# Performance work log

Measured on AMD Instinct MI355X. Metric: run time of the kernel, lower is better.

Reference implementation:

```python
import jax, jax.numpy as jnp
import numpy as np
from math import sqrt

B, C, L = 32, 32, 512            # batch, channels(enc_in), seq_len
INTRA, INTER = 1024, 256          # memory-bank intra_len, inter_len
DCP, DDE = 64, 512                # compress width (retrieved set size), denoise hidden
SCALE = 0.05


def setup_inputs() -> dict:
    key = jax.random.key(0)
    ks = jax.random.split(key, 12)
    s = 0.02  # small init scale for weights
    return {
        "x_loc": jax.random.normal(ks[0], (B, C, L), jnp.float32),
        "indices": jax.random.randint(ks[1], (B, L), 0, INTRA),
        "map_raw": jax.random.normal(ks[2], (C, INTRA, INTER), jnp.float32),
        # compress: Linear(INTER->DCP), ReLU, Linear(DCP->DCP)
        "cW1": jax.random.normal(ks[3], (DCP, INTER), jnp.float32) * s,
        "cb1": jnp.zeros((DCP,), jnp.float32),
        "cW2": jax.random.normal(ks[4], (DCP, DCP), jnp.float32) * s,
        "cb2": jnp.zeros((DCP,), jnp.float32),
        # denoise: Linear(INTRA->DDE), ReLU, Linear(DDE->INTRA)
        "dW1": jax.random.normal(ks[5], (DDE, INTRA), jnp.float32) * s,
        "db1": jnp.zeros((DDE,), jnp.float32),
        "dW2": jax.random.normal(ks[6], (INTRA, DDE), jnp.float32) * s,
        "db2": jnp.zeros((INTRA,), jnp.float32),
        "lamda1": jnp.zeros((C, 1), jnp.float32),
        "lamda2": jnp.zeros((1, L), jnp.float32),
    }


def reference(x_loc, indices, map_raw, cW1, cb1, cW2, cb2,
              dW1, db1, dW2, db2, lamda1, lamda2):
    # compress along inter_len: (C, INTRA, INTER) -> (C, INTRA, DCP)
    map_tmp = jax.nn.relu(map_raw @ cW1.T + cb1) @ cW2.T + cb2
    map_tmp = jnp.swapaxes(map_tmp, 1, 2)            # (C, DCP, INTRA)
    # denoise along intra_len
    map_st = jax.nn.relu(map_tmp @ dW1.T + db1) @ dW2.T + db2  # (C, DCP, INTRA)
    # gather: map_dy[b,c,d,l] = map_st[c, d, indices[b,l]]
    map_dy = jnp.transpose(map_st[:, :, indices], (2, 0, 1, 3))  # (B, C, DCP, L)
    # l1 similarity (negative L1 distance, scaled by sqrt(L))
    scores = -jnp.sum(jnp.abs(x_loc[:, :, None, :] - map_dy), axis=-1) / sqrt(L)  # (B,C,DCP)
    scores = jax.nn.softmax(scores * SCALE, axis=2)
    lamda = jax.nn.sigmoid(lamda1) @ jax.nn.sigmoid(lamda2)     # (C, L)
    x_global = jnp.einsum('bchl,bch->bcl', map_dy, scores)      # (B, C, L)
    return x_global * lamda + x_loc * (1.0 - lamda)
```

## Files before the change

kernel.cpp:

```cpp
#include <hip/hip_runtime.h>
#include <hip/hip_bf16.h>

#define Bn 32
#define Cn 32
#define Ln 512
#define INTRA 1024
#define INTER 256
#define DCP 64
#define DDE 512
#define SCALEF 0.05f

typedef __attribute__((ext_vector_type(8))) short short8;
typedef __attribute__((ext_vector_type(4))) float floatx4;

__device__ __forceinline__ short bf16_of(float f) {
    union { float f; unsigned u; } v; v.f = f;
    unsigned r = (v.u + 0x7FFFu + ((v.u >> 16) & 1u)) >> 16;
    return (short)r;
}
__device__ __forceinline__ float f_of_bf16(short h) {
    union { unsigned u; float f; } v;
    v.u = ((unsigned)(unsigned short)h) << 16;
    return v.f;
}

__global__ __launch_bounds__(256) void prep_weights(
    const float* __restrict__ cW1, const float* __restrict__ cW2,
    const float* __restrict__ dW1, const float* __restrict__ dW2,
    short* __restrict__ cW1b, short* __restrict__ cW2b,
    short* __restrict__ dW1b, short* __restrict__ dW2b)
{
    int i = blockIdx.x * 256 + threadIdx.x;
    if (i < 64 * 256) cW1b[i] = bf16_of(cW1[i]);
    if (i < 64 * 64)  cW2b[i] = bf16_of(cW2[i]);
    if (i < DDE * INTRA) { dW1b[i] = bf16_of(dW1[i]); dW2b[i] = bf16_of(dW2[i]); }
}

__global__ __launch_bounds__(256) void compress_fused(
    const float* __restrict__ map_raw, const short* __restrict__ cW1b,
    const float* __restrict__ cb1, const short* __restrict__ cW2b,
    const float* __restrict__ cb2, short* __restrict__ M1T)
{
    const int c  = blockIdx.y;
    const int m0 = blockIdx.x * 64;
    const float* A = map_raw + (long)c * INTRA * INTER + (long)m0 * INTER;

    __shared__ short lds[64 * 32 + 64 * 32 + 64 * 64];
    short* Asb = lds;
    short* Bsb = lds + 2048;
    short* Tsb = lds + 4096;

    const int t    = threadIdx.x;
    const int w    = t >> 6;
    const int lane = t & 63;
    const int ln   = lane & 15;
    const int quad = lane >> 4;
    const int sr = t >> 2;
    const int sk = (t & 3) * 8;

    floatx4 acc[4] = {};

    float4 a0 = *(const float4*)(A + sr * INTER + sk);
    float4 a1 = *(const float4*)(A + sr * INTER + sk + 4);
    short8 bpre = *(const short8*)(cW1b + sr * INTER + sk);

    for (int k0 = 0; k0 < INTER; k0 += 32) {
        __syncthreads();
        short8 av;
        av[0] = bf16_of(a0.x); av[1] = bf16_of(a0.y);
        av[2] = bf16_of(a0.z); av[3] = bf16_of(a0.w);
        av[4] = bf16_of(a1.x); av[5] = bf16_of(a1.y);
        av[6] = bf16_of(a1.z); av[7] = bf16_of(a1.w);
        *(short8*)&Asb[sr * 32 + sk] = av;
        *(short8*)&Bsb[sr * 32 + sk] = bpre;
        __syncthreads();

        if (k0 + 32 < INTER) {
            a0 = *(const float4*)(A + sr * INTER + k0 + 32 + sk);
            a1 = *(const float4*)(A + sr * INTER + k0 + 32 + sk + 4);
            bpre = *(const short8*)(cW1b + sr * INTER + k0 + 32 + sk);
        }

        short8 af = *(const short8*)&Asb[(w * 16 + ln) * 32 + quad * 8];
        #pragma unroll
        for (int nt = 0; nt < 4; ++nt) {
            short8 bf = *(const short8*)&Bsb[(nt * 16 + ln) * 32 + quad * 8];
            acc[nt] = __builtin_amdgcn_mfma_f32_16x16x32_bf16(af, bf, acc[nt], 0, 0, 0);
        }
    }

    __syncthreads();

    #pragma unroll
    for (int nt = 0; nt < 4; ++nt) {
        const int n = nt * 16 + ln;
        const float b = cb1[n];
        #pragma unroll
        for (int r = 0; r < 4; ++r) {
            const int m = w * 16 + quad * 4 + r;
            Tsb[m * 64 + n] = bf16_of(fmaxf(acc[nt][r] + b, 0.f));
        }
    }
    {
        const int n = t >> 2, kc = (t & 3) * 16;
        *(short8*)&lds[n * 64 + kc]     = *(const short8*)(cW2b + n * 64 + kc);
        *(short8*)&lds[n * 64 + kc + 8] = *(const short8*)(cW2b + n * 64 + kc + 8);
    }
    __syncthreads();

    floatx4 acc2[4] = {};
    #pragma unroll
    for (int ks = 0; ks < 2; ++ks) {
        short8 af = *(const short8*)&Tsb[(w * 16 + ln) * 64 + ks * 32 + quad * 8];
        #pragma unroll
        for (int nt = 0; nt < 4; ++nt) {
            short8 bf = *(const short8*)&lds[(nt * 16 + ln) * 64 + ks * 32 + quad * 8];
            acc2[nt] = __builtin_amdgcn_mfma_f32_16x16x32_bf16(af, bf, acc2[nt], 0, 0, 0);
        }
    }

    short* outp = M1T + (long)c * 64 * INTRA;
    #pragma unroll
    for (int nt = 0; nt < 4; ++nt) {
        const int n = nt * 16 + ln;
        const float b = cb2[n];
        short t0 = bf16_of(acc2[nt][0] + b);
        short t1 = bf16_of(acc2[nt][1] + b);
        short t2 = bf16_of(acc2[nt][2] + b);
        short t3 = bf16_of(acc2[nt][3] + b);
        const int m = m0 + w * 16 + quad * 4;
        *(short4*)(outp + (long)n * INTRA + m) = make_short4(t0, t1, t2, t3);
    }
}

__global__ __launch_bounds__(256) void gemm_dn1(
    const short* __restrict__ A, const short* __restrict__ M1T,
    const float* __restrict__ db1, short* __restrict__ HT)
{
    const int c  = blockIdx.y;
    const int m0 = blockIdx.x * 64;
    const short* Bc = M1T + (long)c * 64 * INTRA;

    __shared__ short Asb[64 * 72];
    __shared__ short Bsb[64 * 72];

    const int t = threadIdx.x, w = t >> 6, lane = t & 63;
    const int ln = lane & 15, quad = lane >> 4;
    const int sr = t >> 2, sk = (t & 3) * 16;

    floatx4 acc[4] = {};
    short8 a0 = *(const short8*)(A + (long)(m0 + sr) * INTRA + sk);
    short8 a1 = *(const short8*)(A + (long)(m0 + sr) * INTRA + sk + 8);
    short8 b0 = *(const short8*)(Bc + (long)sr * INTRA + sk);
    short8 b1 = *(const short8*)(Bc + (long)sr * INTRA + sk + 8);

    for (int k0 = 0; k0 < INTRA; k0 += 64) {
        __syncthreads();
        *(short8*)&Asb[sr * 72 + sk]     = a0;
        *(short8*)&Asb[sr * 72 + sk + 8] = a1;
        *(short8*)&Bsb[sr * 72 + sk]     = b0;
        *(short8*)&Bsb[sr * 72 + sk + 8] = b1;
        __syncthreads();
        const int kn = k0 + 64;
        if (kn < INTRA) {
            a0 = *(const short8*)(A + (long)(m0 + sr) * INTRA + kn + sk);
            a1 = *(const short8*)(A + (long)(m0 + sr) * INTRA + kn + sk + 8);
            b0 = *(const short8*)(Bc + (long)sr * INTRA + kn + sk);
            b1 = *(const short8*)(Bc + (long)sr * INTRA + kn + sk + 8);
        }
        short8 af0 = *(const short8*)&Asb[(w * 16 + ln) * 72 + quad * 8];
        short8 af1 = *(const short8*)&Asb[(w * 16 + ln) * 72 + 32 + quad * 8];
        #pragma unroll
        for (int nt = 0; nt < 4; ++nt) {
            short8 bf0 = *(const short8*)&Bsb[(nt * 16 + ln) * 72 + quad * 8];
            short8 bf1 = *(const short8*)&Bsb[(nt * 16 + ln) * 72 + 32 + quad * 8];
            acc[nt] = __builtin_amdgcn_mfma_f32_16x16x32_bf16(af0, bf0, acc[nt], 0, 0, 0);
            acc[nt] = __builtin_amdgcn_mfma_f32_16x16x32_bf16(af1, bf1, acc[nt], 0, 0, 0);
        }
    }

    float bm[4];
    #pragma unroll
    for (int r = 0; r < 4; ++r) bm[r] = db1[m0 + w * 16 + quad * 4 + r];

    short* outp = HT + (long)c * 64 * DDE;
    #pragma unroll
    for (int nt = 0; nt < 4; ++nt) {
        const int n = nt * 16 + ln;
        float v0 = fmaxf(acc[nt][0] + bm[0], 0.f);
        float v1 = fmaxf(acc[nt][1] + bm[1], 0.f);
        float v2 = fmaxf(acc[nt][2] + bm[2], 0.f);
        float v3 = fmaxf(acc[nt][3] + bm[3], 0.f);
        const int m = m0 + w * 16 + quad * 4;
        *(short4*)(outp + (long)n * DDE + m) =
            make_short4(bf16_of(v0), bf16_of(v1), bf16_of(v2), bf16_of(v3));
    }
}

__global__ __launch_bounds__(256) void gemm_dn2(
    const short* __restrict__ HT, const short* __restrict__ dW2b,
    const float* __restrict__ db2, short* __restrict__ S16)
{
    const int c  = blockIdx.y;
    const int n0 = blockIdx.x * 64;
    const short* A = HT + (long)c * 64 * DDE;
    const short* B = dW2b + (long)n0 * DDE;

    __shared__ short Asb[64 * 72];
    __shared__ short Bsb[64 * 72];

    const int t = threadIdx.x, w = t >> 6, lane = t & 63;
    const int ln = lane & 15, quad = lane >> 4;
    const int sr = t >> 2, sk = (t & 3) * 16;

    floatx4 acc[4] = {};
    short8 a0 = *(const short8*)(A + (long)sr * DDE + sk);
    short8 a1 = *(const short8*)(A + (long)sr * DDE + sk + 8);
    short8 b0 = *(const short8*)(B + (long)sr * DDE + sk);
    short8 b1 = *(const short8*)(B + (long)sr * DDE + sk + 8);

    for (int k0 = 0; k0 < DDE; k0 += 64) {
        __syncthreads();
        *(short8*)&Asb[sr * 72 + sk]     = a0;
        *(short8*)&Asb[sr * 72 + sk + 8] = a1;
        *(short8*)&Bsb[sr * 72 + sk]     = b0;
        *(short8*)&Bsb[sr * 72 + sk + 8] = b1;
        __syncthreads();
        const int kn = k0 + 64;
        if (kn < DDE) {
            a0 = *(const short8*)(A + (long)sr * DDE + kn + sk);
            a1 = *(const short8*)(A + (long)sr * DDE + kn + sk + 8);
            b0 = *(const short8*)(B + (long)sr * DDE + kn + sk);
            b1 = *(const short8*)(B + (long)sr * DDE + kn + sk + 8);
        }
        short8 af0 = *(const short8*)&Asb[(w * 16 + ln) * 72 + quad * 8];
        short8 af1 = *(const short8*)&Asb[(w * 16 + ln) * 72 + 32 + quad * 8];
        #pragma unroll
        for (int nt = 0; nt < 4; ++nt) {
            short8 bf0 = *(const short8*)&Bsb[(nt * 16 + ln) * 72 + quad * 8];
            short8 bf1 = *(const short8*)&Bsb[(nt * 16 + ln) * 72 + 32 + quad * 8];
            acc[nt] = __builtin_amdgcn_mfma_f32_16x16x32_bf16(af0, bf0, acc[nt], 0, 0, 0);
            acc[nt] = __builtin_amdgcn_mfma_f32_16x16x32_bf16(af1, bf1, acc[nt], 0, 0, 0);
        }
    }

    #pragma unroll
    for (int nt = 0; nt < 4; ++nt) {
        const int n = n0 + nt * 16 + ln;
        const float bb = db2[n];
        const int m = w * 16 + quad * 4;
        short t0 = bf16_of(acc[nt][0] + bb);
        short t1 = bf16_of(acc[nt][1] + bb);
        short t2 = bf16_of(acc[nt][2] + bb);
        short t3 = bf16_of(acc[nt][3] + bb);
        *(short4*)(S16 + ((long)c * INTRA + n) * DCP + m) = make_short4(t0, t1, t2, t3);
    }
}

__global__ __launch_bounds__(256) void fuse_kernel(
    const float* __restrict__ x_loc, const int* __restrict__ indices,
    const short* __restrict__ S16, const float* __restrict__ lamda1,
    const float* __restrict__ lamda2, float* __restrict__ out)
{
    const int c = blockIdx.x;
    const int b = blockIdx.y;

    __shared__ float xs[Ln];
    __shared__ int   idx[Ln];
    __shared__ float red[4][DCP];
    __shared__ short wbf[DCP];
    __shared__ float ob[Ln];

    const int t = threadIdx.x;
    const float* xp = x_loc + ((long)b * Cn + c) * Ln;
    const int*   ip = indices + (long)b * Ln;
    ((float2*)xs)[t] = ((const float2*)xp)[t];
    ((int2*)idx)[t]  = ((const int2*)ip)[t];
    __syncthreads();

    const short* Sc = S16 + (long)c * INTRA * DCP;
    const int lane = t & 63;
    const int w    = t >> 6;
    const int r    = lane >> 4;
    const int dg   = lane & 15;

    float s0 = 0.f, s1 = 0.f, s2 = 0.f, s3 = 0.f;
    #pragma unroll 4
    for (int i = 0; i < 32; ++i) {
        const int lbase = w * 128 + i * 4;
        const int row   = idx[lbase + r];
        short4 g = *(const short4*)(Sc + (long)row * DCP + dg * 4);
        const float x = xs[lbase + r];
        s0 += fabsf(x - f_of_bf16(g.x));
        s1 += fabsf(x - f_of_bf16(g.y));
        s2 += fabsf(x - f_of_bf16(g.z));
        s3 += fabsf(x - f_of_bf16(g.w));
    }
    s0 += __shfl_xor(s0, 16); s0 += __shfl_xor(s0, 32);
    s1 += __shfl_xor(s1, 16); s1 += __shfl_xor(s1, 32);
    s2 += __shfl_xor(s2, 16); s2 += __shfl_xor(s2, 32);
    s3 += __shfl_xor(s3, 16); s3 += __shfl_xor(s3, 32);
    if (lane < 16) {
        red[w][dg * 4 + 0] = s0;
        red[w][dg * 4 + 1] = s1;
        red[w][dg * 4 + 2] = s2;
        red[w][dg * 4 + 3] = s3;
    }
    __syncthreads();

    if (t < DCP) {
        float sc = red[0][t] + red[1][t] + red[2][t] + red[3][t];
        sc = -sc * (SCALEF * 0.044194173824159216f);
        float m = sc;
        #pragma unroll
        for (int o = 32; o > 0; o >>= 1) m = fmaxf(m, __shfl_xor(m, o));
        float e = __expf(sc - m);
        float ssum = e;
        #pragma unroll
        for (int o = 32; o > 0; o >>= 1) ssum += __shfl_xor(ssum, o);
        wbf[t] = bf16_of(e / ssum);
    }
    __syncthreads();

    const int quad = lane >> 4;
    const int ln16 = lane & 15;
    short8 bw0 = *(const short8*)&wbf[quad * 8];
    short8 bw1 = *(const short8*)&wbf[32 + quad * 8];

    #pragma unroll
    for (int mt = 0; mt < 8; ++mt) {
        const int mrow = w * 128 + mt * 16 + ln16;
        const short* rp = Sc + (long)idx[mrow] * DCP;
        short8 a0 = *(const short8*)(rp + quad * 8);
        short8 a1 = *(const short8*)(rp + 32 + quad * 8);
        floatx4 acc = {};
        acc = __builtin_amdgcn_mfma_f32_16x16x32_bf16(a0, bw0, acc, 0, 0, 0);
        acc = __builtin_amdgcn_mfma_f32_16x16x32_bf16(a1, bw1, acc, 0, 0, 0);
        if (ln16 == 0) {
            const int l0 = w * 128 + mt * 16 + quad * 4;
            ob[l0 + 0] = acc[0];
            ob[l0 + 1] = acc[1];
            ob[l0 + 2] = acc[2];
            ob[l0 + 3] = acc[3];
        }
    }
    __syncthreads();

    const float lam1 = 1.f / (1.f + __expf(-lamda1[c]));
    #pragma unroll
    for (int j = 0; j < 2; ++j) {
        const int l = t + j * 256;
        const float lam = lam1 * (1.f / (1.f + __expf(-lamda2[l])));
        out[((long)b * Cn + c) * Ln + l] = ob[l] * lam + xs[l] * (1.f - lam);
    }
}

extern "C" void kernel_launch(void* const* d_in, const int* in_sizes, int n_in,
                              void* d_out, int out_size, void* d_ws, size_t ws_size,
                              hipStream_t stream)
{
    const float* x_loc   = (const float*)d_in[0];
    const int*   indices = (const int*)d_in[1];
    const float* map_raw = (const float*)d_in[2];
    const float* cW1     = (const float*)d_in[3];
    const float* cb1     = (const float*)d_in[4];
    const float* cW2     = (const float*)d_in[5];
    const float* cb2     = (const float*)d_in[6];
    const float* dW1     = (const float*)d_in[7];
    const float* db1     = (const float*)d_in[8];
    const float* dW2     = (const float*)d_in[9];
    const float* db2     = (const float*)d_in[10];
    const float* lamda1  = (const float*)d_in[11];
    const float* lamda2  = (const float*)d_in[12];
    float* out = (float*)d_out;

    short* wsS  = (short*)d_ws;
    short* cW1b = wsS;
    short* cW2b = cW1b + 16384;
    short* dW1b = cW2b + 4096;
    short* dW2b = dW1b + 524288;
    short* M1T  = dW2b + 524288;
    short* HT   = M1T + 2097152;
    short* S16  = HT + 1048576;

    prep_weights<<<2048, 256, 0, stream>>>(cW1, cW2, dW1, dW2,
                                           cW1b, cW2b, dW1b, dW2b);

    compress_fused<<<dim3(INTRA / 64, Cn), 256, 0, stream>>>(
        map_raw, cW1b, cb1, cW2b, cb2, M1T);

    gemm_dn1<<<dim3(DDE / 64, Cn), 256, 0, stream>>>(
        dW1b, M1T, db1, HT);

    gemm_dn2<<<dim3(INTRA / 64, Cn), 256, 0, stream>>>(
        HT, dW2b, db2, S16);

    fuse_kernel<<<dim3(Cn, Bn), 256, 0, stream>>>(
        x_loc, indices, S16, lamda1, lamda2, out);
}
```

Measured before the change: 141.8 us.

## Replace LDS-staged GEMMs with per-wave register double-buffered MFMA loads

Rewrites the compress, dn1 and dn2 GEMM kernels so that each wave loads its MFMA fragments straight from global memory into a two-deep register prefetch buffer. This removes the LDS staging and the __syncthreads barriers in the k-loops. gemm_dn2 now gives each wave a 16x128 output tile, cutting the grid to a quarter of its former size and reusing the A fragment across eight MFMAs. The trade is redundant global/L2 traffic, because waves in a block no longer share tiles through LDS, plus higher register pressure and fewer blocks for dn2.

```diff
diff --git a/kernel.cpp b/kernel.cpp
--- a/kernel.cpp
+++ b/kernel.cpp
@@ -41,80 +41,72 @@
     const float* __restrict__ cb1, const short* __restrict__ cW2b,
     const float* __restrict__ cb2, short* __restrict__ M1T)
 {
-    const int c  = blockIdx.y;
-    const int m0 = blockIdx.x * 64;
-    const float* A = map_raw + (long)c * INTRA * INTER + (long)m0 * INTER;
-
-    __shared__ short lds[64 * 32 + 64 * 32 + 64 * 64];
-    short* Asb = lds;
-    short* Bsb = lds + 2048;
-    short* Tsb = lds + 4096;
-
+    const int c    = blockIdx.y;
     const int t    = threadIdx.x;
     const int w    = t >> 6;
     const int lane = t & 63;
     const int ln   = lane & 15;
     const int quad = lane >> 4;
-    const int sr = t >> 2;
-    const int sk = (t & 3) * 8;
+    const int m0   = blockIdx.x * 64 + w * 16;
+
+    const float* Ap = map_raw + ((long)c * INTRA + m0) * INTER + (long)ln * INTER + quad * 8;
+
+    __shared__ short Ts[4][16 * 64];
 
     floatx4 acc[4] = {};
 
-    float4 a0 = *(const float4*)(A + sr * INTER + sk);
-    float4 a1 = *(const float4*)(A + sr * INTER + sk + 4);
-    short8 bpre = *(const short8*)(cW1b + sr * INTER + sk);
-
-    for (int k0 = 0; k0 < INTER; k0 += 32) {
-        __syncthreads();
+    float4 pa0[2], pa1[2];
+    short8 pb[2][4];
+    #pragma unroll
+    for (int ib = 0; ib < 2; ++ib) {
+        const int kk = ib * 32;
+        pa0[ib] = *(const float4*)(Ap + kk);
+        pa1[ib] = *(const float4*)(Ap + kk + 4);
+        #pragma unroll
+        for (int nt = 0; nt < 4; ++nt)
+            pb[ib][nt] = *(const short8*)(cW1b + (nt * 16 + ln) * INTER + kk + quad * 8);
+    }
+
+    int ib = 0;
+    for (int k0 = 0; k0 < INTER; k0 += 32, ib ^= 1) {
+        float4 c0 = pa0[ib], c1 = pa1[ib];
+        short8 bc0 = pb[ib][0], bc1 = pb[ib][1], bc2 = pb[ib][2], bc3 = pb[ib][3];
+        const int kn = k0 + 64;
+        if (kn < INTER) {
+            pa0[ib] = *(const float4*)(Ap + kn);
+            pa1[ib] = *(const float4*)(Ap + kn + 4);
+            #pragma unroll
+            for (int nt = 0; nt < 4; ++nt)
+                pb[ib][nt] = *(const short8*)(cW1b + (nt * 16 + ln) * INTER + kn + quad * 8);
+        }
         short8 av;
-        av[0] = bf16_of(a0.x); av[1] = bf16_of(a0.y);
-        av[2] = bf16_of(a0.z); av[3] = bf16_of(a0.w);
-        av[4] = bf16_of(a1.x); av[5] = bf16_of(a1.y);
-        av[6] = bf16_of(a1.z); av[7] = bf16_of(a1.w);
-        *(short8*)&Asb[sr * 32 + sk] = av;
-        *(short8*)&Bsb[sr * 32 + sk] = bpre;
-        __syncthreads();
-
-        if (k0 + 32 < INTER) {
-            a0 = *(const float4*)(A + sr * INTER + k0 + 32 + sk);
-            a1 = *(const float4*)(A + sr * INTER + k0 + 32 + sk + 4);
-            bpre = *(const short8*)(cW1b + sr * INTER + k0 + 32 + sk);
-        }
-
-        short8 af = *(const short8*)&Asb[(w * 16 + ln) * 32 + quad * 8];
-        #pragma unroll
-        for (int nt = 0; nt < 4; ++nt) {
-            short8 bf = *(const short8*)&Bsb[(nt * 16 + ln) * 32 + quad * 8];
-            acc[nt] = __builtin_amdgcn_mfma_f32_16x16x32_bf16(af, bf, acc[nt], 0, 0, 0);
-        }
-    }
-
-    __syncthreads();
+        av[0] = bf16_of(c0.x); av[1] = bf16_of(c0.y);
+        av[2] = bf16_of(c0.z); av[3] = bf16_of(c0.w);
+        av[4] = bf16_of(c1.x); av[5] = bf16_of(c1.y);
+        av[6] = bf16_of(c1.z); av[7] = bf16_of(c1.w);
+        acc[0] = __builtin_amdgcn_mfma_f32_16x16x32_bf16(av, bc0, acc[0], 0, 0, 0);
+        acc[1] = __builtin_amdgcn_mfma_f32_16x16x32_bf16(av, bc1, acc[1], 0, 0, 0);
+        acc[2] = __builtin_amdgcn_mfma_f32_16x16x32_bf16(av, bc2, acc[2], 0, 0, 0);
+        acc[3] = __builtin_amdgcn_mfma_f32_16x16x32_bf16(av, bc3, acc[3], 0, 0, 0);
+    }
 
     #pragma unroll
     for (int nt = 0; nt < 4; ++nt) {
         const int n = nt * 16 + ln;
         const float b = cb1[n];
         #pragma unroll
-        for (int r = 0; r < 4; ++r) {
-            const int m = w * 16 + quad * 4 + r;
-            Tsb[m * 64 + n] = bf16_of(fmaxf(acc[nt][r] + b, 0.f));
-        }
-    }
-    {
-        const int n = t >> 2, kc = (t & 3) * 16;
-        *(short8*)&lds[n * 64 + kc]     = *(const short8*)(cW2b + n * 64 + kc);
-        *(short8*)&lds[n * 64 + kc + 8] = *(const short8*)(cW2b + n * 64 + kc + 8);
+        for (int r = 0; r < 4; ++r)
+            Ts[w][(quad * 4 + r) * 64 + n] = bf16_of(fmaxf(acc[nt][r] + b, 0.f));
     }
     __syncthreads();
 
     floatx4 acc2[4] = {};
     #pragma unroll
     for (int ks = 0; ks < 2; ++ks) {
-        short8 af = *(const short8*)&Tsb[(w * 16 + ln) * 64 + ks * 32 + quad * 8];
+        short8 af = *(const short8*)&Ts[w][ln * 64 + ks * 32 + quad * 8];
         #pragma unroll
         for (int nt = 0; nt < 4; ++nt) {
-            short8 bf = *(const short8*)&lds[(nt * 16 + ln) * 64 + ks * 32 + quad * 8];
+            short8 bf = *(const short8*)(cW2b + (nt * 16 + ln) * 64 + ks * 32 + quad * 8);
             acc2[nt] = __builtin_amdgcn_mfma_f32_16x16x32_bf16(af, bf, acc2[nt], 0, 0, 0);
         }
     }
@@ -128,71 +120,67 @@
         short t1 = bf16_of(acc2[nt][1] + b);
         short t2 = bf16_of(acc2[nt][2] + b);
         short t3 = bf16_of(acc2[nt][3] + b);
-        const int m = m0 + w * 16 + quad * 4;
-        *(short4*)(outp + (long)n * INTRA + m) = make_short4(t0, t1, t2, t3);
+        *(short4*)(outp + (long)n * INTRA + m0 + quad * 4) = make_short4(t0, t1, t2, t3);
     }
 }
 
 __global__ __launch_bounds__(256) void gemm_dn1(
-    const short* __restrict__ A, const short* __restrict__ M1T,
+    const short* __restrict__ dW1b, const short* __restrict__ M1T,
     const float* __restrict__ db1, short* __restrict__ HT)
 {
-    const int c  = blockIdx.y;
-    const int m0 = blockIdx.x * 64;
-    const short* Bc = M1T + (long)c * 64 * INTRA;
-
-    __shared__ short Asb[64 * 72];
-    __shared__ short Bsb[64 * 72];
-
-    const int t = threadIdx.x, w = t >> 6, lane = t & 63;
-    const int ln = lane & 15, quad = lane >> 4;
-    const int sr = t >> 2, sk = (t & 3) * 16;
+    const int c    = blockIdx.y;
+    const int t    = threadIdx.x;
+    const int w    = t >> 6;
+    const int lane = t & 63;
+    const int ln   = lane & 15;
+    const int quad = lane >> 4;
+    const int h0   = (blockIdx.x * 4 + w) * 16;
+
+    const short* Ap = dW1b + (long)(h0 + ln) * INTRA + quad * 8;
+    const short* Bp = M1T + (long)c * 64 * INTRA + (long)ln * INTRA + quad * 8;
 
     floatx4 acc[4] = {};
-    short8 a0 = *(const short8*)(A + (long)(m0 + sr) * INTRA + sk);
-    short8 a1 = *(const short8*)(A + (long)(m0 + sr) * INTRA + sk + 8);
-    short8 b0 = *(const short8*)(Bc + (long)sr * INTRA + sk);
-    short8 b1 = *(const short8*)(Bc + (long)sr * INTRA + sk + 8);
-
-    for (int k0 = 0; k0 < INTRA; k0 += 64) {
-        __syncthreads();
-        *(short8*)&Asb[sr * 72 + sk]     = a0;
-        *(short8*)&Asb[sr * 72 + sk + 8] = a1;
-        *(short8*)&Bsb[sr * 72 + sk]     = b0;
-        *(short8*)&Bsb[sr * 72 + sk + 8] = b1;
-        __syncthreads();
+    short8 pa[2];
+    short8 pb[2][4];
+    #pragma unroll
+    for (int ib = 0; ib < 2; ++ib) {
+        const int kk = ib * 32;
+        pa[ib] = *(const short8*)(Ap + kk);
+        #pragma unroll
+        for (int nt = 0; nt < 4; ++nt)
+            pb[ib][nt] = *(const short8*)(Bp + (long)nt * 16 * INTRA + kk);
+    }
+
+    int ib = 0;
+    for (int k0 = 0; k0 < INTRA; k0 += 32, ib ^= 1) {
+        short8 ac = pa[ib];
+        short8 b0 = pb[ib][0], b1 = pb[ib][1], b2 = pb[ib][2], b3 = pb[ib][3];
         const int kn = k0 + 64;
         if (kn < INTRA) {
-            a0 = *(const short8*)(A + (long)(m0 + sr) * INTRA + kn + sk);
-            a1 = *(const short8*)(A + (long)(m0 + sr) * INTRA + kn + sk + 8);
-            b0 = *(const short8*)(Bc + (long)sr * INTRA + kn + sk);
-            b1 = *(const short8*)(Bc + (long)sr * INTRA + kn + sk + 8);
-        }
-        short8 af0 = *(const short8*)&Asb[(w * 16 + ln) * 72 + quad * 8];
-        short8 af1 = *(const short8*)&Asb[(w * 16 + ln) * 72 + 32 + quad * 8];
-        #pragma unroll
-        for (int nt = 0; nt < 4; ++nt) {
-            short8 bf0 = *(const short8*)&Bsb[(nt * 16 + ln) * 72 + quad * 8];
-            short8 bf1 = *(const short8*)&Bsb[(nt * 16 + ln) * 72 + 32 + quad * 8];
-            acc[nt] = __builtin_amdgcn_mfma_f32_16x16x32_bf16(af0, bf0, acc[nt], 0, 0, 0);
-            acc[nt] = __builtin_amdgcn_mfma_f32_16x16x32_bf16(af1, bf1, acc[nt], 0, 0, 0);
-        }
+            pa[ib] = *(const short8*)(Ap + kn);
+            #pragma unroll
+            for (int nt = 0; nt < 4; ++nt)
+                pb[ib][nt] = *(const short8*)(Bp + (long)nt * 16 * INTRA + kn);
+        }
+        acc[0] = __builtin_amdgcn_mfma_f32_16x16x32_bf16(ac, b0, acc[0], 0, 0, 0);
+        acc[1] = __builtin_amdgcn_mfma_f32_16x16x32_bf16(ac, b1, acc[1], 0, 0, 0);
+        acc[2] = __builtin_amdgcn_mfma_f32_16x16x32_bf16(ac, b2, acc[2], 0, 0, 0);
+        acc[3] = __builtin_amdgcn_mfma_f32_16x16x32_bf16(ac, b3, acc[3], 0, 0, 0);
     }
 
     float bm[4];
     #pragma unroll
-    for (int r = 0; r < 4; ++r) bm[r] = db1[m0 + w * 16 + quad * 4 + r];
+    for (int r = 0; r < 4; ++r) bm[r] = db1[h0 + quad * 4 + r];
 
     short* outp = HT + (long)c * 64 * DDE;
     #pragma unroll
     for (int nt = 0; nt < 4; ++nt) {
-        const int n = nt * 16 + ln;
+        const int d = nt * 16 + ln;
         float v0 = fmaxf(acc[nt][0] + bm[0], 0.f);
         float v1 = fmaxf(acc[nt][1] + bm[1], 0.f);
         float v2 = fmaxf(acc[nt][2] + bm[2], 0.f);
         float v3 = fmaxf(acc[nt][3] + bm[3], 0.f);
-        const int m = m0 + w * 16 + quad * 4;
-        *(short4*)(outp + (long)n * DDE + m) =
+        *(short4*)(outp + (long)d * DDE + h0 + quad * 4) =
             make_short4(bf16_of(v0), bf16_of(v1), bf16_of(v2), bf16_of(v3));
     }
 }
@@ -201,59 +189,59 @@
     const short* __restrict__ HT, const short* __restrict__ dW2b,
     const float* __restrict__ db2, short* __restrict__ S16)
 {
-    const int c  = blockIdx.y;
-    const int n0 = blockIdx.x * 64;
-    const short* A = HT + (long)c * 64 * DDE;
-    const short* B = dW2b + (long)n0 * DDE;
-
-    __shared__ short Asb[64 * 72];
-    __shared__ short Bsb[64 * 72];
-
-    const int t = threadIdx.x, w = t >> 6, lane = t & 63;
-    const int ln = lane & 15, quad = lane >> 4;
-    const int sr = t >> 2, sk = (t & 3) * 16;
-
-    floatx4 acc[4] = {};
-    short8 a0 = *(const short8*)(A + (long)sr * DDE + sk);
-    short8 a1 = *(const short8*)(A + (long)sr * DDE + sk + 8);
-    short8 b0 = *(const short8*)(B + (long)sr * DDE + sk);
-    short8 b1 = *(const short8*)(B + (long)sr * DDE + sk + 8);
-
-    for (int k0 = 0; k0 < DDE; k0 += 64) {
-        __syncthreads();
-        *(short8*)&Asb[sr * 72 + sk]     = a0;
-        *(short8*)&Asb[sr * 72 + sk + 8] = a1;
-        *(short8*)&Bsb[sr * 72 + sk]     = b0;
-        *(short8*)&Bsb[sr * 72 + sk + 8] = b1;
-        __syncthreads();
+    const int c    = blockIdx.y;
+    const int t    = threadIdx.x;
+    const int w    = t >> 6;
+    const int lane = t & 63;
+    const int ln   = lane & 15;
+    const int quad = lane >> 4;
+    const int widx = blockIdx.x * 4 + w;
+    const int dt   = widx & 3;
+    const int i0   = (widx >> 2) * 128;
+
+    const short* Ap = HT + (long)c * 64 * DDE + (long)(dt * 16 + ln) * DDE + quad * 8;
+    const short* Bp = dW2b + (long)i0 * DDE + (long)ln * DDE + quad * 8;
+
+    floatx4 acc[8] = {};
+    short8 pa[2];
+    short8 pb[2][8];
+    #pragma unroll
+    for (int ib = 0; ib < 2; ++ib) {
+        const int kk = ib * 32;
+        pa[ib] = *(const short8*)(Ap + kk);
+        #pragma unroll
+        for (int nt = 0; nt < 8; ++nt)
+            pb[ib][nt] = *(const short8*)(Bp + (long)nt * 16 * DDE + kk);
+    }
+
+    int ib = 0;
+    for (int k0 = 0; k0 < DDE; k0 += 32, ib ^= 1) {
+        short8 ac = pa[ib];
+        short8 bc[8];
+        #pragma unroll
+        for (int nt = 0; nt < 8; ++nt) bc[nt] = pb[ib][nt];
         const int kn = k0 + 64;
         if (kn < DDE) {
-            a0 = *(const short8*)(A + (long)sr * DDE + kn + sk);
-            a1 = *(const short8*)(A + (long)sr * DDE + kn + sk + 8);
-            b0 = *(const short8*)(B + (long)sr * DDE + kn + sk);
-            b1 = *(const short8*)(B + (long)sr * DDE + kn + sk + 8);
-        }
-        short8 af0 = *(const short8*)&Asb[(w * 16 + ln) * 72 + quad * 8];
-        short8 af1 = *(const short8*)&Asb[(w * 16 + ln) * 72 + 32 + quad * 8];
-        #pragma unroll
-        for (int nt = 0; nt < 4; ++nt) {
-            short8 bf0 = *(const short8*)&Bsb[(nt * 16 + ln) * 72 + quad * 8];
-            short8 bf1 = *(const short8*)&Bsb[(nt * 16 + ln) * 72 + 32 + quad * 8];
-            acc[nt] = __builtin_amdgcn_mfma_f32_16x16x32_bf16(af0, bf0, acc[nt], 0, 0, 0);
-            acc[nt] = __builtin_amdgcn_mfma_f32_16x16x32_bf16(af1, bf1, acc[nt], 0, 0, 0);
-        }
-    }
-
-    #pragma unroll
-    for (int nt = 0; nt < 4; ++nt) {
-        const int n = n0 + nt * 16 + ln;
-        const float bb = db2[n];
-        const int m = w * 16 + quad * 4;
+            pa[ib] = *(const short8*)(Ap + kn);
+            #pragma unroll
+            for (int nt = 0; nt < 8; ++nt)
+                pb[ib][nt] = *(const short8*)(Bp + (long)nt * 16 * DDE + kn);
+        }
+        #pragma unroll
+        for (int nt = 0; nt < 8; ++nt)
+            acc[nt] = __builtin_amdgcn_mfma_f32_16x16x32_bf16(ac, bc[nt], acc[nt], 0, 0, 0);
+    }
+
+    const int d0 = dt * 16 + quad * 4;
+    #pragma unroll
+    for (int nt = 0; nt < 8; ++nt) {
+        const int i = i0 + nt * 16 + ln;
+        const float bb = db2[i];
         short t0 = bf16_of(acc[nt][0] + bb);
         short t1 = bf16_of(acc[nt][1] + bb);
         short t2 = bf16_of(acc[nt][2] + bb);
         short t3 = bf16_of(acc[nt][3] + bb);
-        *(short4*)(S16 + ((long)c * INTRA + n) * DCP + m) = make_short4(t0, t1, t2, t3);
+        *(short4*)(S16 + ((long)c * INTRA + i) * DCP + d0) = make_short4(t0, t1, t2, t3);
     }
 }
 
@@ -392,7 +380,7 @@
     gemm_dn1<<<dim3(DDE / 64, Cn), 256, 0, stream>>>(
         dW1b, M1T, db1, HT);
 
-    gemm_dn2<<<dim3(INTRA / 64, Cn), 256, 0, stream>>>(
+    gemm_dn2<<<dim3(INTRA / 64 / 4, Cn), 256, 0, stream>>>(
         HT, dW2b, db2, S16);
 
     fuse_kernel<<<dim3(Cn, Bn), 256, 0, stream>>>(
```

After: 165.0 us. 1.16x slower.

## Drop weight-prep kernel; convert fp32 weights to bf16 inside GEMM tile loads

Applied to the files above, without the earlier changes.

Removes the separate prep_weights launch that converted all weight matrices to bf16. Each GEMM now reads the fp32 weights and converts them while staging tiles into LDS. The K-tile depth is raised to 64 or 128 with padded LDS rows, and gemm_dn1 switches to 32-row tiles, doubling its grid. This saves a launch and a round trip through memory for the weights. The cost is that fp32 weights are re-read and re-converted by every block, with more global traffic per block and higher register use.

```diff
diff --git a/kernel.cpp b/kernel.cpp
--- a/kernel.cpp
+++ b/kernel.cpp
@@ -23,72 +23,63 @@
     v.u = ((unsigned)(unsigned short)h) << 16;
     return v.f;
 }
-
-__global__ __launch_bounds__(256) void prep_weights(
-    const float* __restrict__ cW1, const float* __restrict__ cW2,
-    const float* __restrict__ dW1, const float* __restrict__ dW2,
-    short* __restrict__ cW1b, short* __restrict__ cW2b,
-    short* __restrict__ dW1b, short* __restrict__ dW2b)
-{
-    int i = blockIdx.x * 256 + threadIdx.x;
-    if (i < 64 * 256) cW1b[i] = bf16_of(cW1[i]);
-    if (i < 64 * 64)  cW2b[i] = bf16_of(cW2[i]);
-    if (i < DDE * INTRA) { dW1b[i] = bf16_of(dW1[i]); dW2b[i] = bf16_of(dW2[i]); }
+__device__ __forceinline__ short8 cvt8(float4 a, float4 b) {
+    short8 r;
+    r[0] = bf16_of(a.x); r[1] = bf16_of(a.y); r[2] = bf16_of(a.z); r[3] = bf16_of(a.w);
+    r[4] = bf16_of(b.x); r[5] = bf16_of(b.y); r[6] = bf16_of(b.z); r[7] = bf16_of(b.w);
+    return r;
 }
 
 __global__ __launch_bounds__(256) void compress_fused(
-    const float* __restrict__ map_raw, const short* __restrict__ cW1b,
-    const float* __restrict__ cb1, const short* __restrict__ cW2b,
+    const float* __restrict__ map_raw, const float* __restrict__ cW1,
+    const float* __restrict__ cb1, const float* __restrict__ cW2,
     const float* __restrict__ cb2, short* __restrict__ M1T)
 {
     const int c  = blockIdx.y;
     const int m0 = blockIdx.x * 64;
-    const float* A = map_raw + (long)c * INTRA * INTER + (long)m0 * INTER;
-
-    __shared__ short lds[64 * 32 + 64 * 32 + 64 * 64];
-    short* Asb = lds;
-    short* Bsb = lds + 2048;
-    short* Tsb = lds + 4096;
-
-    const int t    = threadIdx.x;
-    const int w    = t >> 6;
-    const int lane = t & 63;
-    const int ln   = lane & 15;
-    const int quad = lane >> 4;
-    const int sr = t >> 2;
-    const int sk = (t & 3) * 8;
+    const float* A = map_raw + ((long)c * INTRA + m0) * INTER;
+
+    __shared__ short Asb[64 * 72];
+    __shared__ short Bsb[64 * 72];
+    __shared__ short Tsb[64 * 72];
+
+    const int t = threadIdx.x, w = t >> 6, lane = t & 63;
+    const int ln = lane & 15, quad = lane >> 4;
+    const int sr = t >> 2, sk = (t & 3) * 16;
+
+    const float* ap = A + sr * INTER + sk;
+    const float* bp = cW1 + sr * INTER + sk;
 
     floatx4 acc[4] = {};
-
-    float4 a0 = *(const float4*)(A + sr * INTER + sk);
-    float4 a1 = *(const float4*)(A + sr * INTER + sk + 4);
-    short8 bpre = *(const short8*)(cW1b + sr * INTER + sk);
-
-    for (int k0 = 0; k0 < INTER; k0 += 32) {
-        __syncthreads();
-        short8 av;
-        av[0] = bf16_of(a0.x); av[1] = bf16_of(a0.y);
-        av[2] = bf16_of(a0.z); av[3] = bf16_of(a0.w);
-        av[4] = bf16_of(a1.x); av[5] = bf16_of(a1.y);
-        av[6] = bf16_of(a1.z); av[7] = bf16_of(a1.w);
-        *(short8*)&Asb[sr * 32 + sk] = av;
-        *(short8*)&Bsb[sr * 32 + sk] = bpre;
-        __syncthreads();
-
-        if (k0 + 32 < INTER) {
-            a0 = *(const float4*)(A + sr * INTER + k0 + 32 + sk);
-            a1 = *(const float4*)(A + sr * INTER + k0 + 32 + sk + 4);
-            bpre = *(const short8*)(cW1b + sr * INTER + k0 + 32 + sk);
-        }
-
-        short8 af = *(const short8*)&Asb[(w * 16 + ln) * 32 + quad * 8];
-        #pragma unroll
-        for (int nt = 0; nt < 4; ++nt) {
-            short8 bf = *(const short8*)&Bsb[(nt * 16 + ln) * 32 + quad * 8];
-            acc[nt] = __builtin_amdgcn_mfma_f32_16x16x32_bf16(af, bf, acc[nt], 0, 0, 0);
-        }
-    }
-
+    float4 a0 = *(const float4*)(ap),     a1 = *(const float4*)(ap + 4);
+    float4 a2 = *(const float4*)(ap + 8), a3 = *(const float4*)(ap + 12);
+    float4 b0 = *(const float4*)(bp),     b1 = *(const float4*)(bp + 4);
+    float4 b2 = *(const float4*)(bp + 8), b3 = *(const float4*)(bp + 12);
+
+    for (int k0 = 0; k0 < INTER; k0 += 64) {
+        __syncthreads();
+        *(short8*)&Asb[sr * 72 + sk]     = cvt8(a0, a1);
+        *(short8*)&Asb[sr * 72 + sk + 8] = cvt8(a2, a3);
+        *(short8*)&Bsb[sr * 72 + sk]     = cvt8(b0, b1);
+        *(short8*)&Bsb[sr * 72 + sk + 8] = cvt8(b2, b3);
+        __syncthreads();
+        const int kn = k0 + 64;
+        if (kn < INTER) {
+            a0 = *(const float4*)(ap + kn);     a1 = *(const float4*)(ap + kn + 4);
+            a2 = *(const float4*)(ap + kn + 8); a3 = *(const float4*)(ap + kn + 12);
+            b0 = *(const float4*)(bp + kn);     b1 = *(const float4*)(bp + kn + 4);
+            b2 = *(const float4*)(bp + kn + 8); b3 = *(const float4*)(bp + kn + 12);
+        }
+        #pragma unroll
+        for (int kc = 0; kc < 2; ++kc) {
+            short8 af = *(const short8*)&Asb[(w * 16 + ln) * 72 + kc * 32 + quad * 8];
+            #pragma unroll
+            for (int nt = 0; nt < 4; ++nt) {
+                short8 bf = *(const short8*)&Bsb[(nt * 16 + ln) * 72 + kc * 32 + quad * 8];
+                acc[nt] = __builtin_amdgcn_mfma_f32_16x16x32_bf16(af, bf, acc[nt], 0, 0, 0);
+            }
+        }
+    }
     __syncthreads();
 
     #pragma unroll
@@ -96,25 +87,19 @@
         const int n = nt * 16 + ln;
         const float b = cb1[n];
         #pragma unroll
-        for (int r = 0; r < 4; ++r) {
-            const int m = w * 16 + quad * 4 + r;
-            Tsb[m * 64 + n] = bf16_of(fmaxf(acc[nt][r] + b, 0.f));
-        }
-    }
-    {
-        const int n = t >> 2, kc = (t & 3) * 16;
-        *(short8*)&lds[n * 64 + kc]     = *(const short8*)(cW2b + n * 64 + kc);
-        *(short8*)&lds[n * 64 + kc + 8] = *(const short8*)(cW2b + n * 64 + kc + 8);
+        for (int r = 0; r < 4; ++r)
+            Tsb[(w * 16 + quad * 4 + r) * 72 + n] = bf16_of(fmaxf(acc[nt][r] + b, 0.f));
     }
     __syncthreads();
 
     floatx4 acc2[4] = {};
     #pragma unroll
     for (int ks = 0; ks < 2; ++ks) {
-        short8 af = *(const short8*)&Tsb[(w * 16 + ln) * 64 + ks * 32 + quad * 8];
+        short8 af = *(const short8*)&Tsb[(w * 16 + ln) * 72 + ks * 32 + quad * 8];
         #pragma unroll
         for (int nt = 0; nt < 4; ++nt) {
-            short8 bf = *(const short8*)&lds[(nt * 16 + ln) * 64 + ks * 32 + quad * 8];
+            const float* wp = cW2 + (nt * 16 + ln) * 64 + ks * 32 + quad * 8;
+            short8 bf = cvt8(*(const float4*)wp, *(const float4*)(wp + 4));
             acc2[nt] = __builtin_amdgcn_mfma_f32_16x16x32_bf16(af, bf, acc2[nt], 0, 0, 0);
         }
     }
@@ -128,132 +113,147 @@
         short t1 = bf16_of(acc2[nt][1] + b);
         short t2 = bf16_of(acc2[nt][2] + b);
         short t3 = bf16_of(acc2[nt][3] + b);
-        const int m = m0 + w * 16 + quad * 4;
-        *(short4*)(outp + (long)n * INTRA + m) = make_short4(t0, t1, t2, t3);
+        *(short4*)(outp + (long)n * INTRA + m0 + w * 16 + quad * 4) =
+            make_short4(t0, t1, t2, t3);
     }
 }
 
 __global__ __launch_bounds__(256) void gemm_dn1(
-    const short* __restrict__ A, const short* __restrict__ M1T,
+    const float* __restrict__ dW1, const short* __restrict__ M1T,
     const float* __restrict__ db1, short* __restrict__ HT)
 {
     const int c  = blockIdx.y;
-    const int m0 = blockIdx.x * 64;
-    const short* Bc = M1T + (long)c * 64 * INTRA;
-
-    __shared__ short Asb[64 * 72];
-    __shared__ short Bsb[64 * 72];
+    const int h0 = blockIdx.x * 32;
+
+    __shared__ short Asb[32 * 136];
+    __shared__ short Bsb[64 * 136];
 
     const int t = threadIdx.x, w = t >> 6, lane = t & 63;
     const int ln = lane & 15, quad = lane >> 4;
-    const int sr = t >> 2, sk = (t & 3) * 16;
-
-    floatx4 acc[4] = {};
-    short8 a0 = *(const short8*)(A + (long)(m0 + sr) * INTRA + sk);
-    short8 a1 = *(const short8*)(A + (long)(m0 + sr) * INTRA + sk + 8);
-    short8 b0 = *(const short8*)(Bc + (long)sr * INTRA + sk);
-    short8 b1 = *(const short8*)(Bc + (long)sr * INTRA + sk + 8);
-
-    for (int k0 = 0; k0 < INTRA; k0 += 64) {
-        __syncthreads();
-        *(short8*)&Asb[sr * 72 + sk]     = a0;
-        *(short8*)&Asb[sr * 72 + sk + 8] = a1;
-        *(short8*)&Bsb[sr * 72 + sk]     = b0;
-        *(short8*)&Bsb[sr * 72 + sk + 8] = b1;
-        __syncthreads();
-        const int kn = k0 + 64;
+    const int ar = t >> 3, ak = (t & 7) * 16;
+    const int br = t >> 2, bk = (t & 3) * 32;
+
+    const float* Ap = dW1 + (long)(h0 + ar) * INTRA + ak;
+    const short* Bp = M1T + (long)c * 64 * INTRA + (long)br * INTRA + bk;
+
+    floatx4 acc[2] = {};
+    float4 fa0 = *(const float4*)(Ap),     fa1 = *(const float4*)(Ap + 4);
+    float4 fa2 = *(const float4*)(Ap + 8), fa3 = *(const float4*)(Ap + 12);
+    short8 sb0 = *(const short8*)(Bp),      sb1 = *(const short8*)(Bp + 8);
+    short8 sb2 = *(const short8*)(Bp + 16), sb3 = *(const short8*)(Bp + 24);
+
+    const int mb = (w & 1) * 16;
+    const int nb = (w >> 1) * 2;
+
+    for (int k0 = 0; k0 < INTRA; k0 += 128) {
+        __syncthreads();
+        *(short8*)&Asb[ar * 136 + ak]      = cvt8(fa0, fa1);
+        *(short8*)&Asb[ar * 136 + ak + 8]  = cvt8(fa2, fa3);
+        *(short8*)&Bsb[br * 136 + bk]      = sb0;
+        *(short8*)&Bsb[br * 136 + bk + 8]  = sb1;
+        *(short8*)&Bsb[br * 136 + bk + 16] = sb2;
+        *(short8*)&Bsb[br * 136 + bk + 24] = sb3;
+        __syncthreads();
+        const int kn = k0 + 128;
         if (kn < INTRA) {
-            a0 = *(const short8*)(A + (long)(m0 + sr) * INTRA + kn + sk);
-            a1 = *(const short8*)(A + (long)(m0 + sr) * INTRA + kn + sk + 8);
-            b0 = *(const short8*)(Bc + (long)sr * INTRA + kn + sk);
-            b1 = *(const short8*)(Bc + (long)sr * INTRA + kn + sk + 8);
-        }
-        short8 af0 = *(const short8*)&Asb[(w * 16 + ln) * 72 + quad * 8];
-        short8 af1 = *(const short8*)&Asb[(w * 16 + ln) * 72 + 32 + quad * 8];
-        #pragma unroll
-        for (int nt = 0; nt < 4; ++nt) {
-            short8 bf0 = *(const short8*)&Bsb[(nt * 16 + ln) * 72 + quad * 8];
-            short8 bf1 = *(const short8*)&Bsb[(nt * 16 + ln) * 72 + 32 + quad * 8];
-            acc[nt] = __builtin_amdgcn_mfma_f32_16x16x32_bf16(af0, bf0, acc[nt], 0, 0, 0);
-            acc[nt] = __builtin_amdgcn_mfma_f32_16x16x32_bf16(af1, bf1, acc[nt], 0, 0, 0);
+            fa0 = *(const float4*)(Ap + kn);     fa1 = *(const float4*)(Ap + kn + 4);
+            fa2 = *(const float4*)(Ap + kn + 8); fa3 = *(const float4*)(Ap + kn + 12);
+            sb0 = *(const short8*)(Bp + kn);      sb1 = *(const short8*)(Bp + kn + 8);
+            sb2 = *(const short8*)(Bp + kn + 16); sb3 = *(const short8*)(Bp + kn + 24);
+        }
+        #pragma unroll
+        for (int kc = 0; kc < 4; ++kc) {
+            short8 af  = *(const short8*)&Asb[(mb + ln) * 136 + kc * 32 + quad * 8];
+            short8 bf0 = *(const short8*)&Bsb[((nb + 0) * 16 + ln) * 136 + kc * 32 + quad * 8];
+            short8 bf1 = *(const short8*)&Bsb[((nb + 1) * 16 + ln) * 136 + kc * 32 + quad * 8];
+            acc[0] = __builtin_amdgcn_mfma_f32_16x16x32_bf16(af, bf0, acc[0], 0, 0, 0);
+            acc[1] = __builtin_amdgcn_mfma_f32_16x16x32_bf16(af, bf1, acc[1], 0, 0, 0);
         }
     }
 
     float bm[4];
     #pragma unroll
-    for (int r = 0; r < 4; ++r) bm[r] = db1[m0 + w * 16 + quad * 4 + r];
+    for (int r = 0; r < 4; ++r) bm[r] = db1[h0 + mb + quad * 4 + r];
 
     short* outp = HT + (long)c * 64 * DDE;
     #pragma unroll
-    for (int nt = 0; nt < 4; ++nt) {
-        const int n = nt * 16 + ln;
-        float v0 = fmaxf(acc[nt][0] + bm[0], 0.f);
-        float v1 = fmaxf(acc[nt][1] + bm[1], 0.f);
-        float v2 = fmaxf(acc[nt][2] + bm[2], 0.f);
-        float v3 = fmaxf(acc[nt][3] + bm[3], 0.f);
-        const int m = m0 + w * 16 + quad * 4;
-        *(short4*)(outp + (long)n * DDE + m) =
+    for (int j = 0; j < 2; ++j) {
+        const int d = (nb + j) * 16 + ln;
+        float v0 = fmaxf(acc[j][0] + bm[0], 0.f);
+        float v1 = fmaxf(acc[j][1] + bm[1], 0.f);
+        float v2 = fmaxf(acc[j][2] + bm[2], 0.f);
+        float v3 = fmaxf(acc[j][3] + bm[3], 0.f);
+        *(short4*)(outp + (long)d * DDE + h0 + mb + quad * 4) =
             make_short4(bf16_of(v0), bf16_of(v1), bf16_of(v2), bf16_of(v3));
     }
 }
 
 __global__ __launch_bounds__(256) void gemm_dn2(
-    const short* __restrict__ HT, const short* __restrict__ dW2b,
+    const short* __restrict__ HT, const float* __restrict__ dW2,
     const float* __restrict__ db2, short* __restrict__ S16)
 {
     const int c  = blockIdx.y;
     const int n0 = blockIdx.x * 64;
-    const short* A = HT + (long)c * 64 * DDE;
-    const short* B = dW2b + (long)n0 * DDE;
-
-    __shared__ short Asb[64 * 72];
-    __shared__ short Bsb[64 * 72];
+
+    __shared__ short Asb[64 * 136];
+    __shared__ short Bsb[64 * 136];
 
     const int t = threadIdx.x, w = t >> 6, lane = t & 63;
     const int ln = lane & 15, quad = lane >> 4;
-    const int sr = t >> 2, sk = (t & 3) * 16;
+    const int ar = t >> 2, ak = (t & 3) * 32;
+
+    const short* Ap = HT + (long)c * 64 * DDE + (long)ar * DDE + ak;
+    const float* Bp = dW2 + (long)(n0 + ar) * DDE + ak;
 
     floatx4 acc[4] = {};
-    short8 a0 = *(const short8*)(A + (long)sr * DDE + sk);
-    short8 a1 = *(const short8*)(A + (long)sr * DDE + sk + 8);
-    short8 b0 = *(const short8*)(B + (long)sr * DDE + sk);
-    short8 b1 = *(const short8*)(B + (long)sr * DDE + sk + 8);
-
-    for (int k0 = 0; k0 < DDE; k0 += 64) {
-        __syncthreads();
-        *(short8*)&Asb[sr * 72 + sk]     = a0;
-        *(short8*)&Asb[sr * 72 + sk + 8] = a1;
-        *(short8*)&Bsb[sr * 72 + sk]     = b0;
-        *(short8*)&Bsb[sr * 72 + sk + 8] = b1;
-        __syncthreads();
-        const int kn = k0 + 64;
+    short8 sa0 = *(const short8*)(Ap),      sa1 = *(const short8*)(Ap + 8);
+    short8 sa2 = *(const short8*)(Ap + 16), sa3 = *(const short8*)(Ap + 24);
+    float4 fb0 = *(const float4*)(Bp),      fb1 = *(const float4*)(Bp + 4);
+    float4 fb2 = *(const float4*)(Bp + 8),  fb3 = *(const float4*)(Bp + 12);
+    float4 fb4 = *(const float4*)(Bp + 16), fb5 = *(const float4*)(Bp + 20);
+    float4 fb6 = *(const float4*)(Bp + 24), fb7 = *(const float4*)(Bp + 28);
+
+    for (int k0 = 0; k0 < DDE; k0 += 128) {
+        __syncthreads();
+        *(short8*)&Asb[ar * 136 + ak]      = sa0;
+        *(short8*)&Asb[ar * 136 + ak + 8]  = sa1;
+        *(short8*)&Asb[ar * 136 + ak + 16] = sa2;
+        *(short8*)&Asb[ar * 136 + ak + 24] = sa3;
+        *(short8*)&Bsb[ar * 136 + ak]      = cvt8(fb0, fb1);
+        *(short8*)&Bsb[ar * 136 + ak + 8]  = cvt8(fb2, fb3);
+        *(short8*)&Bsb[ar * 136 + ak + 16] = cvt8(fb4, fb5);
+        *(short8*)&Bsb[ar * 136 + ak + 24] = cvt8(fb6, fb7);
+        __syncthreads();
+        const int kn = k0 + 128;
         if (kn < DDE) {
-            a0 = *(const short8*)(A + (long)sr * DDE + kn + sk);
-            a1 = *(const short8*)(A + (long)sr * DDE + kn + sk + 8);
-            b0 = *(const short8*)(B + (long)sr * DDE + kn + sk);
-            b1 = *(const short8*)(B + (long)sr * DDE + kn + sk + 8);
-        }
-        short8 af0 = *(const short8*)&Asb[(w * 16 + ln) * 72 + quad * 8];
-        short8 af1 = *(const short8*)&Asb[(w * 16 + ln) * 72 + 32 + quad * 8];
-        #pragma unroll
-        for (int nt = 0; nt < 4; ++nt) {
-            short8 bf0 = *(const short8*)&Bsb[(nt * 16 + ln) * 72 + quad * 8];
-            short8 bf1 = *(const short8*)&Bsb[(nt * 16 + ln) * 72 + 32 + quad * 8];
-            acc[nt] = __builtin_amdgcn_mfma_f32_16x16x32_bf16(af0, bf0, acc[nt], 0, 0, 0);
-            acc[nt] = __builtin_amdgcn_mfma_f32_16x16x32_bf16(af1, bf1, acc[nt], 0, 0, 0);
-        }
-    }
-
+            sa0 = *(const short8*)(Ap + kn);      sa1 = *(const short8*)(Ap + kn + 8);
+            sa2 = *(const short8*)(Ap + kn + 16); sa3 = *(const short8*)(Ap + kn + 24);
+            fb0 = *(const float4*)(Bp + kn);      fb1 = *(const float4*)(Bp + kn + 4);
+            fb2 = *(const float4*)(Bp + kn + 8);  fb3 = *(const float4*)(Bp + kn + 12);
+            fb4 = *(const float4*)(Bp + kn + 16); fb5 = *(const float4*)(Bp + kn + 20);
+            fb6 = *(const float4*)(Bp + kn + 24); fb7 = *(const float4*)(Bp + kn + 28);
+        }
+        #pragma unroll
+        for (int kc = 0; kc < 4; ++kc) {
+            short8 af = *(const short8*)&Asb[(w * 16 + ln) * 136 + kc * 32 + quad * 8];
+            #pragma unroll
+            for (int nt = 0; nt < 4; ++nt) {
+                short8 bf = *(const short8*)&Bsb[(nt * 16 + ln) * 136 + kc * 32 + quad * 8];
+                acc[nt] = __builtin_amdgcn_mfma_f32_16x16x32_bf16(af, bf, acc[nt], 0, 0, 0);
+            }
+        }
+    }
+
+    const int d0 = w * 16 + quad * 4;
     #pragma unroll
     for (int nt = 0; nt < 4; ++nt) {
-        const int n = n0 + nt * 16 + ln;
-        const float bb = db2[n];
-        const int m = w * 16 + quad * 4;
+        const int i = n0 + nt * 16 + ln;
+        const float bb = db2[i];
         short t0 = bf16_of(acc[nt][0] + bb);
         short t1 = bf16_of(acc[nt][1] + bb);
         short t2 = bf16_of(acc[nt][2] + bb);
         short t3 = bf16_of(acc[nt][3] + bb);
-        *(short4*)(S16 + ((long)c * INTRA + n) * DCP + m) = make_short4(t0, t1, t2, t3);
+        *(short4*)(S16 + ((long)c * INTRA + i) * DCP + d0) = make_short4(t0, t1, t2, t3);
     }
 }
 
@@ -374,26 +374,19 @@
     const float* lamda2  = (const float*)d_in[12];
     float* out = (float*)d_out;
 
-    short* wsS  = (short*)d_ws;
-    short* cW1b = wsS;
-    short* cW2b = cW1b + 16384;
-    short* dW1b = cW2b + 4096;
-    short* dW2b = dW1b + 524288;
-    short* M1T  = dW2b + 524288;
-    short* HT   = M1T + 2097152;
-    short* S16  = HT + 1048576;
-
-    prep_weights<<<2048, 256, 0, stream>>>(cW1, cW2, dW1, dW2,
-                                           cW1b, cW2b, dW1b, dW2b);
+    short* wsS = (short*)d_ws;
+    short* M1T = wsS;
+    short* HT  = M1T + 2097152;
+    short* S16 = HT + 1048576;
 
     compress_fused<<<dim3(INTRA / 64, Cn), 256, 0, stream>>>(
-        map_raw, cW1b, cb1, cW2b, cb2, M1T);
-
-    gemm_dn1<<<dim3(DDE / 64, Cn), 256, 0, stream>>>(
-        dW1b, M1T, db1, HT);
+        map_raw, cW1, cb1, cW2, cb2, M1T);
+
+    gemm_dn1<<<dim3(DDE / 32, Cn), 256, 0, stream>>>(
+        dW1, M1T, db1, HT);
 
     gemm_dn2<<<dim3(INTRA / 64, Cn), 256, 0, stream>>>(
-        HT, dW2b, db2, S16);
+        HT, dW2, db2, S16);
 
     fuse_kernel<<<dim3(Cn, Bn), 256, 0, stream>>>(
         x_loc, indices, S16, lamda1, lamda2, out);
```

Result: slower. 144.8 us (+2.1%).
